# Kernel tuning notes

Hardware: AMD Instinct MI355X
Metric: run time of the kernel (lower is better)

## Reference

```python
import jax, jax.numpy as jnp
import numpy as np

NUM_HEADS = 16


def setup_inputs() -> dict:
    key = jax.random.key(0)
    ks = jax.random.split(key, 8)
    B, N, C = 2, 1024, 1024
    H, D = NUM_HEADS, C // NUM_HEADS
    Npast = 8192
    s = 0.02
    return {
        "x": jax.random.normal(ks[0], (B, N, C), jnp.float32),
        "past_k": jax.random.normal(ks[1], (B, H, Npast, D), jnp.float32),
        "past_v": jax.random.normal(ks[2], (B, H, Npast, D), jnp.float32),
        "qkv_w": jax.random.normal(ks[3], (3 * C, C), jnp.float32) * s,
        "qkv_b": jax.random.normal(ks[4], (3 * C,), jnp.float32) * s,
        "proj_w": jax.random.normal(ks[5], (C, C), jnp.float32) * s,
        "proj_b": jax.random.normal(ks[6], (C,), jnp.float32) * s,
        "cache_budget": 4096,
    }


def reference(x, past_k, past_v, qkv_w, qkv_b, proj_w, proj_b, cache_budget):
    B, N, C = x.shape
    H = NUM_HEADS
    D = C // H
    scale = D ** -0.5

    # fused QKV projection -> [3, B, H, N, D]
    qkv = (x @ qkv_w.T + qkv_b).reshape(B, N, 3, H, D).transpose(2, 0, 3, 1, 4)
    q, k, v = qkv[0], qkv[1], qkv[2]

    # use_cache path: anchor tokens = current-frame token count on first call
    num_anchor = N
    k = jnp.concatenate([past_k, k], axis=2)  # [B,H,Ntot,D]
    v = jnp.concatenate([past_v, v], axis=2)
    Ntot = k.shape[2]

    # eviction: mean cosine-similarity scoring over candidate (non-anchor) keys.
    # mean_j cos(k_i, k_j) == khat_i . mean_j(khat_j) -- O(N*D), no NxN matrix.
    num_keep = cache_budget - num_anchor
    cand_k = k[:, :, num_anchor:, :]  # [B,H,Ncand,D]
    khat = cand_k / (jnp.linalg.norm(cand_k, axis=-1, keepdims=True) + 1e-6)
    mean_dir = khat.mean(axis=2, keepdims=True)
    mean_scores = (khat * mean_dir).sum(-1)  # [B,H,Ncand]
    # keep the least-redundant tokens (lowest mean similarity)
    _, top_idx = jax.lax.top_k(-mean_scores, num_keep)  # [B,H,num_keep]
    top_idx = jnp.sort(top_idx, axis=-1)
    avg_scores = mean_scores.mean()

    anchor_idx = jnp.broadcast_to(jnp.arange(num_anchor)[None, None, :], (B, H, num_anchor))
    keep_idx = jnp.concatenate([anchor_idx, top_idx + num_anchor], axis=2)  # [B,H,budget]
    gidx = keep_idx[..., None]
    k_new = jnp.take_along_axis(k, jnp.broadcast_to(gidx, (B, H, cache_budget, D)), axis=2)
    v_new = jnp.take_along_axis(v, jnp.broadcast_to(gidx, (B, H, cache_budget, D)), axis=2)

    # SDPA
    logits = jnp.einsum("bhqd,bhkd->bhqk", q, k_new) * scale
    attn = jax.nn.softmax(logits, axis=-1)
    o = jnp.einsum("bhqk,bhkd->bhqd", attn, v_new)
    o = o.transpose(0, 2, 1, 3).reshape(B, N, C)
    out = o @ proj_w.T + proj_b
    return out, k_new, v_new, avg_scores
```

## Files before the change

### kernel.cpp

```cpp
#include <hip/hip_runtime.h>
#include <hip/hip_bf16.h>
#include <math.h>

#define BB 2
#define HH 16
#define NN 1024
#define CC 1024
#define DD 64
#define NPAST 8192
#define NANCH 1024
#define CBUD 4096
#define NKEEP 3072
#define NCAND 8192
#define BH 32

#define TILEB 16384

#define OUT_SZ   (BB*NN*CC)
#define KNEW_OFF ((size_t)OUT_SZ)
#define KNEW_SZ  ((size_t)BH*CBUD*DD)
#define VNEW_OFF (KNEW_OFF + KNEW_SZ)
#define AVG_OFF  (VNEW_OFF + KNEW_SZ)

#define WS_KF   ((size_t)0)
#define WS_VF   ((size_t)2097152)
#define WS_VTS  ((size_t)0)
#define WS_XT   ((size_t)4194304)
#define WS_OT   ((size_t)4194304)
#define WS_WQVT ((size_t)5242880)
#define WS_WPT  ((size_t)5242880)
#define WS_QB   ((size_t)6291456)
#define WS_MD   ((size_t)7340032)
#define WS_SC   ((size_t)7342080)
#define WS_BS   ((size_t)7604224)
#define WS_SEL  ((size_t)7604288)
#define WS_MDP  ((size_t)7702592)
#define WS_BSP  ((size_t)7718976)

typedef __attribute__((ext_vector_type(8))) short short8;
typedef __attribute__((ext_vector_type(4))) float f32x4;

typedef unsigned int __attribute__((address_space(3))) lds_uint;
typedef unsigned int __attribute__((address_space(1))) glb_uint;

__device__ __forceinline__ void gload16(const void* g, void* l) {
    __builtin_amdgcn_global_load_lds((const glb_uint*)g, (lds_uint*)l, 16, 0, 0);
}

__device__ inline unsigned short f2bf(float f) {
    unsigned u = __float_as_uint(f);
    unsigned r = (u + 0x7FFFu + ((u >> 16) & 1u)) >> 16;
    return (unsigned short)r;
}
__device__ inline unsigned cvtpk(float a, float b) {
    __hip_bfloat162 h = __float22bfloat162_rn(make_float2(a, b));
    return *reinterpret_cast<unsigned*>(&h);
}
__device__ __forceinline__ float fexp2(float x) {
#if __has_builtin(__builtin_amdgcn_exp2f)
    return __builtin_amdgcn_exp2f(x);
#else
    return exp2f(x);
#endif
}

__global__ __launch_bounds__(256) void conv_tile(const float* __restrict__ src,
                                                 unsigned short* __restrict__ dst)
{
    int gid = blockIdx.x * 256 + threadIdx.x;
    int r = gid >> 7, k0 = (gid & 127) * 8;
    float4 a = *(const float4*)&src[(size_t)r * 1024 + k0];
    float4 b = *(const float4*)&src[(size_t)r * 1024 + k0 + 4];
    uint4 u;
    u.x = cvtpk(a.x, a.y); u.y = cvtpk(a.z, a.w);
    u.z = cvtpk(b.x, b.y); u.w = cvtpk(b.z, b.w);
    size_t tile = (size_t)(r >> 7) * 16 + (k0 >> 6);
    int inner = (((r & 127) * 128 + (k0 & 63) * 2)) ^ ((r & 7) << 4);
    *(uint4*)((char*)dst + tile * TILEB + inner) = u;
}

__global__ __launch_bounds__(256) void conv_wqv(const float* __restrict__ src,
                                                unsigned short* __restrict__ dst)
{
    int gid = blockIdx.x * 256 + threadIdx.x;
    int n = gid >> 7, k0 = (gid & 127) * 8;
    int srow = (n < 1024) ? n : n + 1024;
    float4 a = *(const float4*)&src[(size_t)srow * 1024 + k0];
    float4 b = *(const float4*)&src[(size_t)srow * 1024 + k0 + 4];
    uint4 u;
    u.x = cvtpk(a.x, a.y); u.y = cvtpk(a.z, a.w);
    u.z = cvtpk(b.x, b.y); u.w = cvtpk(b.z, b.w);
    size_t tile = (size_t)(n >> 7) * 16 + (k0 >> 6);
    int inner = (((n & 127) * 128 + (k0 & 63) * 2)) ^ ((n & 7) << 4);
    *(uint4*)((char*)dst + tile * TILEB + inner) = u;
}

__global__ __launch_bounds__(256) void kf_gemm(const float* __restrict__ x,
                                               const float* __restrict__ w,
                                               const float* __restrict__ bias,
                                               float* __restrict__ ws)
{
    __shared__ float As[16][68];
    __shared__ float Bs[16][68];
    int tid = threadIdx.x;
    int m0 = blockIdx.y * 64;
    int n0 = blockIdx.x * 64;
    int tx = tid & 15, ty = tid >> 4;
    int lr = tid >> 2;
    int lk = (tid & 3) * 4;
    float acc[4][4] = {{0.f}};

    float4 a = *(const float4*)&x[(size_t)(m0 + lr) * CC + lk];
    float4 b = *(const float4*)&w[(size_t)(1024 + n0 + lr) * CC + lk];

    for (int k0 = 0; k0 < CC; k0 += 16) {
        __syncthreads();
        As[lk+0][lr] = a.x; As[lk+1][lr] = a.y; As[lk+2][lr] = a.z; As[lk+3][lr] = a.w;
        Bs[lk+0][lr] = b.x; Bs[lk+1][lr] = b.y; Bs[lk+2][lr] = b.z; Bs[lk+3][lr] = b.w;
        __syncthreads();
        if (k0 + 16 < CC) {
            a = *(const float4*)&x[(size_t)(m0 + lr) * CC + k0 + 16 + lk];
            b = *(const float4*)&w[(size_t)(1024 + n0 + lr) * CC + k0 + 16 + lk];
        }
        float tacc[4][4] = {{0.f}};
        #pragma unroll
        for (int kk = 0; kk < 16; ++kk) {
            float4 a4 = *(const float4*)&As[kk][ty*4];
            float4 b4 = *(const float4*)&Bs[kk][tx*4];
            float av[4] = {a4.x, a4.y, a4.z, a4.w};
            float bv[4] = {b4.x, b4.y, b4.z, b4.w};
            #pragma unroll
            for (int i = 0; i < 4; ++i)
                #pragma unroll
                for (int j = 0; j < 4; ++j)
                    tacc[i][j] += av[i] * bv[j];
        }
        #pragma unroll
        for (int i = 0; i < 4; ++i)
            #pragma unroll
            for (int j = 0; j < 4; ++j)
                acc[i][j] += tacc[i][j];
    }

    int cn0 = n0 + tx * 4;
    int h = cn0 >> 6, dd0 = cn0 & 63;
    float4 b4 = *(const float4*)&bias[1024 + cn0];
    float* kf = ws + WS_KF;
    #pragma unroll
    for (int i = 0; i < 4; ++i) {
        int m = m0 + ty * 4 + i;
        int b2 = m >> 10, n = m & 1023;
        float4 t;
        t.x = acc[i][0] + b4.x; t.y = acc[i][1] + b4.y;
        t.z = acc[i][2] + b4.z; t.w = acc[i][3] + b4.w;
        *(float4*)&kf[(((size_t)b2*HH + h)*NN + n)*DD + dd0] = t;
    }
}

template<int MODE>
__global__ __launch_bounds__(256) void mfma_gemm(const unsigned short* __restrict__ At,
                                                 const unsigned short* __restrict__ Bt,
                                                 const float* __restrict__ bias,
                                                 float* __restrict__ outp)
{
    __shared__ char lds[131072];
    int tid = threadIdx.x;
    int w = tid >> 6, lane = tid & 63;
    int g = lane >> 4, r16 = lane & 15;
    int wr = w >> 1, wc = w & 1;
    int bm = blockIdx.y, bn = blockIdx.x;
    const int KB = 16;
    const float QSCL = 0.125f * 1.44269504089f;

    f32x4 acc[4][4];
    #pragma unroll
    for (int i = 0; i < 4; ++i)
        #pragma unroll
        for (int j = 0; j < 4; ++j) acc[i][j] = 0.f;

    const char* Abase = (const char*)At + (size_t)bm * KB * TILEB;
    const char* Bbase = (const char*)Bt + (size_t)bn * KB * TILEB;

    #pragma unroll
    for (int i = 0; i < 4; ++i) {
        gload16(Abase + (size_t)w*4096 + i*1024 + lane*16, lds + w*4096 + i*1024);
        gload16(Bbase + (size_t)w*4096 + i*1024 + lane*16, lds + TILEB + w*4096 + i*1024);
    }
    asm volatile("s_waitcnt vmcnt(0)" ::: "memory");
    __syncthreads();

    int cur = 0;
    for (int kb = 0; kb < KB; ++kb) {
        char* Acur = lds + cur * (2*TILEB);
        char* Bcur = Acur + TILEB;
        if (kb + 1 < KB) {
            char* Anxt = lds + (cur ^ 1) * (2*TILEB);
            char* Bnxt = Anxt + TILEB;
            const char* an = Abase + (size_t)(kb+1)*TILEB + w*4096;
            const char* bsrc = Bbase + (size_t)(kb+1)*TILEB + w*4096;
            #pragma unroll
            for (int i = 0; i < 4; ++i) {
                gload16(an + i*1024 + lane*16, Anxt + w*4096 + i*1024);
                gload16(bsrc + i*1024 + lane*16, Bnxt + w*4096 + i*1024);
            }
        }
        short8 a0[4], a1[4], b0[4], b1[4];
        #pragma unroll
        for (int mi = 0; mi < 4; ++mi) {
            int row = wr*64 + mi*16 + r16;
            int sw = (row & 7) << 4;
            a0[mi] = *(const short8*)(Acur + ((row*128 + g*16) ^ sw));
            a1[mi] = *(const short8*)(Acur + ((row*128 + 64 + g*16) ^ sw));
        }
        #pragma unroll
        for (int ni = 0; ni < 4; ++ni) {
            int row = wc*64 + ni*16 + r16;
            int sw = (row & 7) << 4;
            b0[ni] = *(const short8*)(Bcur + ((row*128 + g*16) ^ sw));
            b1[ni] = *(const short8*)(Bcur + ((row*128 + 64 + g*16) ^ sw));
        }
        __builtin_amdgcn_s_setprio(1);
        #pragma unroll
        for (int mi = 0; mi < 4; ++mi)
            #pragma unroll
            for (int ni = 0; ni < 4; ++ni) {
                acc[mi][ni] = __builtin_amdgcn_mfma_f32_16x16x32_bf16(a0[mi], b0[ni], acc[mi][ni], 0, 0, 0);
                acc[mi][ni] = __builtin_amdgcn_mfma_f32_16x16x32_bf16(a1[mi], b1[ni], acc[mi][ni], 0, 0, 0);
            }
        __builtin_amdgcn_s_setprio(0);
        asm volatile("s_waitcnt vmcnt(0)" ::: "memory");
        __syncthreads();
        cur ^= 1;
    }

    int nq = bn*128 + wc*64;
    float bv[4];
    #pragma unroll
    for (int ni = 0; ni < 4; ++ni) {
        int n = nq + ni*16 + r16;
        bv[ni] = (MODE == 0) ? bias[(n < 1024) ? n : (n + 1024)] : bias[n];
    }
    #pragma unroll
    for (int mi = 0; mi < 4; ++mi) {
        #pragma unroll
        for (int rr = 0; rr < 4; ++rr) {
            int ml = wr*64 + mi*16 + 4*g + rr;
            int mg = bm*128 + ml;
            int bb = mg >> 10, tok = mg & 1023;
            #pragma unroll
            for (int ni = 0; ni < 4; ++ni) {
                int n = nq + ni*16 + r16;
                float v = acc[mi][ni][rr] + bv[ni];
                if (MODE == 0) {
                    if (n < 1024) {
                        unsigned short* qb = (unsigned short*)(outp + WS_QB);
                        int hh = n >> 6, d = n & 63;
                        qb[(((size_t)bb*16 + hh)*1024 + tok)*64 + d] = f2bf(v * QSCL);
                    } else {
                        float* vf = outp + WS_VF;
                        int hh = (n - 1024) >> 6, d = n & 63;
                        vf[(((size_t)bb*16 + hh)*1024 + tok)*64 + d] = v;
                    }
                } else {
                    outp[(size_t)mg*1024 + n] = v;
                }
            }
        }
    }
}

__global__ __launch_bounds__(256) void meandir_part(const float* __restrict__ past_k,
                                                    float* __restrict__ ws)
{
    int bh = blockIdx.x, seg = blockIdx.y, tid = threadIdx.x;
    const float* kpast = past_k + (size_t)bh * NPAST * DD;
    const float* knew  = ws + WS_KF + (size_t)bh * NN * DD;
    float dir[64];
    #pragma unroll
    for (int i = 0; i < 64; ++i) dir[i] = 0.f;

    int j0 = seg * 1024;
    for (int jj = tid; jj < 1024; jj += 256) {
        int pos = NANCH + j0 + jj;
        const float* row = (pos < NPAST) ? (kpast + (size_t)pos * DD)
                                         : (knew + (size_t)(pos - NPAST) * DD);
        float v[64]; float ss = 0.f;
        #pragma unroll
        for (int g = 0; g < 16; ++g) {
            float4 t = *(const float4*)&row[g*4];
            v[4*g]=t.x; v[4*g+1]=t.y; v[4*g+2]=t.z; v[4*g+3]=t.w;
            ss += t.x*t.x + t.y*t.y + t.z*t.z + t.w*t.w;
        }
        float inv = 1.0f / (sqrtf(ss) + 1e-6f);
        #pragma unroll
        for (int i = 0; i < 64; ++i) dir[i] += v[i] * inv;
    }
    #pragma unroll
    for (int i = 0; i < 64; ++i)
        for (int off = 32; off; off >>= 1) dir[i] += __shfl_xor(dir[i], off);

    __shared__ float sdir[4][64];
    int lane = tid & 63, wid = tid >> 6;
    if (lane == 0) {
        #pragma unroll
        for (int i = 0; i < 64; ++i) sdir[wid][i] = dir[i];
    }
    __syncthreads();
    if (tid < 64) {
        float s = sdir[0][tid] + sdir[1][tid] + sdir[2][tid] + sdir[3][tid];
        ws[WS_MDP + ((size_t)bh*8 + seg)*DD + tid] = s;
    }
}

__global__ void meandir_red(float* __restrict__ ws)
{
    int bh = blockIdx.x, tid = threadIdx.x;
    float s = 0.f;
    #pragma unroll
    for (int seg = 0; seg < 8; ++seg)
        s += ws[WS_MDP + ((size_t)bh*8 + seg)*DD + tid];
    ws[WS_MD + (size_t)bh*DD + tid] = s * (1.0f / (float)NCAND);
}

__global__ __launch_bounds__(256) void scores_part(const float* __restrict__ past_k,
                                                   float* __restrict__ ws)
{
    __shared__ float md[64];
    __shared__ float sred[4];
    int bh = blockIdx.x, seg = blockIdx.y, tid = threadIdx.x;
    if (tid < 64) md[tid] = ws[WS_MD + (size_t)bh*DD + tid];
    __syncthreads();
    const float* kpast = past_k + (size_t)bh * NPAST * DD;
    const float* knew  = ws + WS_KF + (size_t)bh * NN * DD;
    float ssum = 0.f;
    int j0 = seg * 1024;
    for (int jj = tid; jj < 1024; jj += 256) {
        int j = j0 + jj;
        int pos = NANCH + j;
        const float* row = (pos < NPAST) ? (kpast + (size_t)pos * DD)
                                         : (knew + (size_t)(pos - NPAST) * DD);
        float ss = 0.f, dp = 0.f;
        #pragma unroll
        for (int g = 0; g < 16; ++g) {
            float4 t = *(const float4*)&row[g*4];
            ss += t.x*t.x + t.y*t.y + t.z*t.z + t.w*t.w;
            dp += t.x*md[4*g] + t.y*md[4*g+1] + t.z*md[4*g+2] + t.w*md[4*g+3];
        }
        float sc = dp / (sqrtf(ss) + 1e-6f);
        ws[WS_SC + (size_t)bh*NCAND + j] = sc;
        ssum += sc;
    }
    for (int off = 32; off; off >>= 1) ssum += __shfl_xor(ssum, off);
    int lane = tid & 63, wid = tid >> 6;
    if (lane == 0) sred[wid] = ssum;
    __syncthreads();
    if (tid == 0)
        ws[WS_BSP + (size_t)bh*8 + seg] = sred[0] + sred[1] + sred[2] + sred[3];
}

__global__ void avg_k(const float* __restrict__ ws, float* __restrict__ dout)
{
    __shared__ float red[4];
    int tid = threadIdx.x;
    float v = ws[WS_BSP + tid];
    for (int off = 32; off; off >>= 1) v += __shfl_xor(v, off);
    int lane = tid & 63, wid = tid >> 6;
    if (lane == 0) red[wid] = v;
    __syncthreads();
    if (tid == 0)
        dout[AVG_OFF] = (red[0]+red[1]+red[2]+red[3]) * (1.0f / ((float)BH * (float)NCAND));
}

__global__ __launch_bounds__(1024) void topk_k(float* __restrict__ ws, int* __restrict__ sel)
{
    __shared__ unsigned keys[NCAND];
    __shared__ int hist[256];
    __shared__ int red[16];
    __shared__ int red2[16];
    __shared__ int bcast;
    __shared__ unsigned bbyte;
    int bh = blockIdx.x, tid = threadIdx.x;
    int lane = tid & 63, wid = tid >> 6;

    for (int j = tid; j < NCAND; j += 1024) {
        unsigned u = __float_as_uint(ws[WS_SC + (size_t)bh*NCAND + j]);
        u ^= (u & 0x80000000u) ? 0xFFFFFFFFu : 0x80000000u;
        keys[j] = u;
    }
    __syncthreads();

    int rem = NKEEP;
    unsigned prefix = 0;
    #pragma unroll
    for (int pass = 0; pass < 4; ++pass) {
        int shift = 24 - 8*pass;
        if (tid < 256) hist[tid] = 0;
        __syncthreads();
        unsigned himask = (pass == 0) ? 0u : (0xFFFFFFFFu << (shift + 8));
        for (int j = tid; j < NCAND; j += 1024) {
            unsigned k = keys[j];
            if ((k & himask) == prefix)
                atomicAdd(&hist[(k >> shift) & 255], 1);
        }
        __syncthreads();
        if (tid == 0) {
            int cum = 0, b = 0;
            for (; b < 255; ++b) {
                if (rem <= cum + hist[b]) break;
                cum += hist[b];
            }
            bcast = cum;
            bbyte = (unsigned)b;
        }
        __syncthreads();
        rem -= bcast;
        prefix |= (bbyte << shift);
        __syncthreads();
    }
    unsigned T = prefix;

    {
        int cnt = 0;
        for (int j = tid; j < NCAND; j += 1024) cnt += (int)(keys[j] < T);
        for (int off = 32; off; off >>= 1) cnt += __shfl_xor(cnt, off);
        if (lane == 0) red[wid] = cnt;
        __syncthreads();
        if (tid == 0) { int c = 0; for (int i = 0; i < 16; ++i) c += red[i]; bcast = c; }
        __syncthreads();
    }
    int c_less = bcast;
    int ttie = NKEEP - c_less;

    int base = tid * 8;
    unsigned kv[8]; int lcnt = 0, ecnt = 0;
    #pragma unroll
    for (int i = 0; i < 8; ++i) {
        kv[i] = keys[base + i];
        lcnt += (int)(kv[i] < T);
        ecnt += (int)(kv[i] == T);
    }
    int li = lcnt, ei = ecnt;
    for (int off = 1; off < 64; off <<= 1) {
        int tl = __shfl_up(li, off);
        int te = __shfl_up(ei, off);
        if (lane >= off) { li += tl; ei += te; }
    }
    __syncthreads();
    if (lane == 63) { red[wid] = li; red2[wid] = ei; }
    __syncthreads();
    int lb = 0, eb = 0;
    for (int w = 0; w < wid; ++w) { lb += red[w]; eb += red2[w]; }
    lb += li - lcnt; eb += ei - ecnt;
    #pragma unroll
    for (int i = 0; i < 8; ++i) {
        bool less = kv[i] < T, eq = kv[i] == T;
        if (less || (eq && eb < ttie)) {
            int pos = lb + (eb < ttie ? eb : ttie);
            sel[(size_t)bh*NKEEP + pos] = base + i;
        }
        lb += (int)less; eb += (int)eq;
    }
}

__global__ __launch_bounds__(256) void gather_k(const float* __restrict__ past_k,
                                                const float* __restrict__ past_v,
                                                const float* __restrict__ ws,
                                                const int* __restrict__ sel,
                                                float* __restrict__ dout)
{
    int gid = blockIdx.x * 256 + threadIdx.x;
    int row = gid >> 4, lane = gid & 15;
    int bh = row >> 12, r = row & 4095;
    int pos = (r < NANCH) ? r : (NANCH + sel[(size_t)bh*NKEEP + (r - NANCH)]);
    const float *kr, *vr;
    if (pos < NPAST) {
        kr = past_k + ((size_t)bh*NPAST + pos) * DD;
        vr = past_v + ((size_t)bh*NPAST + pos) * DD;
    } else {
        kr = ws + WS_KF + ((size_t)bh*NN + (pos - NPAST)) * DD;
        vr = ws + WS_VF + ((size_t)bh*NN + (pos - NPAST)) * DD;
    }
    float4 kq = *(const float4*)&kr[lane*4];
    float4 vq = *(const float4*)&vr[lane*4];
    *(float4*)&dout[KNEW_OFF + ((size_t)bh*CBUD + r)*DD + lane*4] = kq;
    *(float4*)&dout[VNEW_OFF + ((size_t)bh*CBUD + r)*DD + lane*4] = vq;
}

__global__ __launch_bounds__(256) void vtrans_k(const float* __restrict__ dout,
                                                unsigned short* __restrict__ vt)
{
    __shared__ unsigned short S[64][65];
    int bh = blockIdx.x >> 6, kt = blockIdx.x & 63;
    int c0 = kt * 64;
    int tid = threadIdx.x;
    int r = tid >> 2, c4 = (tid & 3) * 16;
    const float* src = dout + VNEW_OFF + ((size_t)bh*CBUD + c0 + r)*DD + c4;
    #pragma unroll
    for (int i = 0; i < 4; ++i) {
        float4 f = *(const float4*)&src[i*4];
        S[r][c4 + i*4 + 0] = f2bf(f.x);
        S[r][c4 + i*4 + 1] = f2bf(f.y);
        S[r][c4 + i*4 + 2] = f2bf(f.z);
        S[r][c4 + i*4 + 3] = f2bf(f.w);
    }
    __syncthreads();
    int d = r, k4 = c4;
    uint4 u0, u1;
    u0.x = (unsigned)S[k4+0][d] | ((unsigned)S[k4+1][d] << 16);
    u0.y = (unsigned)S[k4+2][d] | ((unsigned)S[k4+3][d] << 16);
    u0.z = (unsigned)S[k4+4][d] | ((unsigned)S[k4+5][d] << 16);
    u0.w = (unsigned)S[k4+6][d] | ((unsigned)S[k4+7][d] << 16);
    u1.x = (unsigned)S[k4+8][d] | ((unsigned)S[k4+9][d] << 16);
    u1.y = (unsigned)S[k4+10][d] | ((unsigned)S[k4+11][d] << 16);
    u1.z = (unsigned)S[k4+12][d] | ((unsigned)S[k4+13][d] << 16);
    u1.w = (unsigned)S[k4+14][d] | ((unsigned)S[k4+15][d] << 16);
    size_t tbase = ((size_t)bh*64 + kt) * 8192;
    int sw = (d & 7) << 4;
    *(uint4*)((char*)vt + tbase + ((d*128 + k4*2)      ^ sw)) = u0;
    *(uint4*)((char*)vt + tbase + ((d*128 + k4*2 + 16) ^ sw)) = u1;
}

__global__ __launch_bounds__(256) void attn_mfma(const unsigned short* __restrict__ qb,
                                                 const float* __restrict__ dout,
                                                 const unsigned short* __restrict__ vt,
                                                 unsigned short* __restrict__ ot)
{
    __shared__ char kls[2][8192];
    __shared__ char vls[2][8192];
    __shared__ char pls[4][2048];

    int orig = blockIdx.x;
    int bid = (orig & 7) * 64 + (orig >> 3);
    int bh = bid >> 4, qt = bid & 15;
    int b = bh >> 4, h = bh & 15;
    int tid = threadIdx.x;
    int w = tid >> 6, lane = tid & 63;
    int g = lane >> 4, r16 = lane & 15;
    int q0 = qt * 64 + w * 16;

    const unsigned short* qrow = qb + ((size_t)bh*NN + q0 + r16) * DD;
    short8 qa0 = *(const short8*)&qrow[8*g];
    short8 qa1 = *(const short8*)&qrow[32 + 8*g];

    const float* kf = dout + KNEW_OFF + (size_t)bh * CBUD * DD;
    const char* vtt = (const char*)vt + (size_t)bh * 64 * 8192;
    char* plw = pls[w];
    int psw = (r16 & 7) << 4;

    int srA = tid >> 3;
    int srB = srA + 32;
    int scb = (tid & 7) * 16;
    int d0  = scb >> 1;
    int sdA = (srA*128 + scb) ^ ((srA & 7) << 4);
    int sdB = (srB*128 + scb) ^ ((srB & 7) << 4);

    f32x4 accd[4];
    #pragma unroll
    for (int dt = 0; dt < 4; ++dt) accd[dt] = 0.f;
    float lsum = 0.f;

    {
        gload16(vtt + tid*16,        vls[0] + tid*16);
        gload16(vtt + 4096 + tid*16, vls[0] + 4096 + tid*16);
        const float* ksA = kf + (size_t)srA * DD + d0;
        const float* ksB = kf + (size_t)srB * DD + d0;
        float4 a0 = *(const float4*)ksA, a1 = *(const float4*)(ksA + 4);
        float4 b0 = *(const float4*)ksB, b1 = *(const float4*)(ksB + 4);
        uint4 kuA, kuB;
        kuA.x = cvtpk(a0.x,a0.y); kuA.y = cvtpk(a0.z,a0.w);
        kuA.z = cvtpk(a1.x,a1.y); kuA.w = cvtpk(a1.z,a1.w);
        kuB.x = cvtpk(b0.x,b0.y); kuB.y = cvtpk(b0.z,b0.w);
        kuB.z = cvtpk(b1.x,b1.y); kuB.w = cvtpk(b1.z,b1.w);
        *(uint4*)&kls[0][sdA] = kuA; *(uint4*)&kls[0][sdB] = kuB;
    }
    __syncthreads();

    int cur = 0;
    for (int t = 0; t < 64; ++t) {
        float4 a0, a1, b0, b1;
        bool more = (t + 1 < 64);
        if (more) {
            gload16(vtt + (size_t)(t+1)*8192 + tid*16,        vls[cur^1] + tid*16);
            gload16(vtt + (size_t)(t+1)*8192 + 4096 + tid*16, vls[cur^1] + 4096 + tid*16);
            const float* ksA = kf + ((size_t)(t+1)*64 + srA) * DD + d0;
            const float* ksB = kf + ((size_t)(t+1)*64 + srB) * DD + d0;
            a0 = *(const float4*)ksA; a1 = *(const float4*)(ksA + 4);
            b0 = *(const float4*)ksB; b1 = *(const float4*)(ksB + 4);
        }

        const char* kb = kls[cur];
        f32x4 sacc[4];
        #pragma unroll
        for (int t4 = 0; t4 < 4; ++t4) sacc[t4] = 0.f;
        __builtin_amdgcn_s_setprio(1);
        #pragma unroll
        for (int t4 = 0; t4 < 4; ++t4) {
            int row = 16*t4 + r16;
            int sw = (r16 & 7) << 4;
            short8 ka0 = *(const short8*)(kb + ((row*128 + g*16) ^ sw));
            short8 ka1 = *(const short8*)(kb + ((row*128 + 64 + g*16) ^ sw));
            sacc[t4] = __builtin_amdgcn_mfma_f32_16x16x32_bf16(ka0, qa0, sacc[t4], 0, 0, 0);
            sacc[t4] = __builtin_amdgcn_mfma_f32_16x16x32_bf16(ka1, qa1, sacc[t4], 0, 0, 0);
        }
        __builtin_amdgcn_s_setprio(0);

        float p[4][4];
        float ps = 0.f;
        #pragma unroll
        for (int t4 = 0; t4 < 4; ++t4) {
            p[t4][0] = fexp2(sacc[t4][0]);
            p[t4][1] = fexp2(sacc[t4][1]);
            p[t4][2] = fexp2(sacc[t4][2]);
            p[t4][3] = fexp2(sacc[t4][3]);
            ps += (p[t4][0] + p[t4][1]) + (p[t4][2] + p[t4][3]);
        }
        lsum += ps;
        #pragma unroll
        for (int t4 = 0; t4 < 4; ++t4) {
            uint2 u;
            u.x = cvtpk(p[t4][0], p[t4][1]);
            u.y = cvtpk(p[t4][2], p[t4][3]);
            int cb = (16*t4 + 4*g) * 2;
            *(uint2*)&plw[(r16*128 + cb) ^ psw] = u;
        }

        short8 pa0 = *(const short8*)&plw[(r16*128 + 16*g)      ^ psw];
        short8 pa1 = *(const short8*)&plw[(r16*128 + 64 + 16*g) ^ psw];
        const char* vb = vls[cur];
        __builtin_amdgcn_s_setprio(1);
        #pragma unroll
        for (int dt = 0; dt < 4; ++dt) {
            int row = dt*16 + r16;
            int sw = (r16 & 7) << 4;
            short8 vb0 = *(const short8*)(vb + ((row*128 + g*16) ^ sw));
            short8 vb1 = *(const short8*)(vb + ((row*128 + 64 + g*16) ^ sw));
            accd[dt] = __builtin_amdgcn_mfma_f32_16x16x32_bf16(pa0, vb0, accd[dt], 0, 0, 0);
            accd[dt] = __builtin_amdgcn_mfma_f32_16x16x32_bf16(pa1, vb1, accd[dt], 0, 0, 0);
        }
        __builtin_amdgcn_s_setprio(0);

        if (more) {
            uint4 kuA, kuB;
            kuA.x = cvtpk(a0.x,a0.y); kuA.y = cvtpk(a0.z,a0.w);
            kuA.z = cvtpk(a1.x,a1.y); kuA.w = cvtpk(a1.z,a1.w);
            kuB.x = cvtpk(b0.x,b0.y); kuB.y = cvtpk(b0.z,b0.w);
            kuB.z = cvtpk(b1.x,b1.y); kuB.w = cvtpk(b1.z,b1.w);
            *(uint4*)&kls[cur^1][sdA] = kuA; *(uint4*)&kls[cur^1][sdB] = kuB;
        }
        __syncthreads();
        cur ^= 1;
    }

    lsum += __shfl_xor(lsum, 16);
    lsum += __shfl_xor(lsum, 32);
    float ivl = 1.0f / lsum;
    float iq[4];
    #pragma unroll
    for (int rr = 0; rr < 4; ++rr) iq[rr] = __shfl(ivl, 20*g + rr);
    #pragma unroll
    for (int dt = 0; dt < 4; ++dt) {
        #pragma unroll
        for (int rr = 0; rr < 4; ++rr) {
            int q = q0 + 4*g + rr;
            int mrow = b*1024 + q;
            int d = dt*16 + r16;
            size_t tile = (size_t)(mrow >> 7) * 16 + h;
            int inner = ((mrow & 127)*128 + d*2) ^ ((mrow & 7) << 4);
            *(unsigned short*)((char*)ot + tile*TILEB + inner) = f2bf(accd[dt][rr] * iq[rr]);
        }
    }
}

extern "C" void kernel_launch(void* const* d_in, const int* in_sizes, int n_in,
                              void* d_out, int out_size, void* d_ws, size_t ws_size,
                              hipStream_t stream)
{
    (void)in_sizes; (void)n_in; (void)out_size; (void)ws_size;
    const float* x      = (const float*)d_in[0];
    const float* past_k = (const float*)d_in[1];
    const float* past_v = (const float*)d_in[2];
    const float* qkv_w  = (const float*)d_in[3];
    const float* qkv_b  = (const float*)d_in[4];
    const float* proj_w = (const float*)d_in[5];
    const float* proj_b = (const float*)d_in[6];
    float* out = (float*)d_out;
    float* ws  = (float*)d_ws;
    int*   sel = (int*)(ws + WS_SEL);
    unsigned short* xt   = (unsigned short*)(ws + WS_XT);
    unsigned short* wqvt = (unsigned short*)(ws + WS_WQVT);
    unsigned short* wpt  = (unsigned short*)(ws + WS_WPT);
    unsigned short* qbp  = (unsigned short*)(ws + WS_QB);
    unsigned short* vtp  = (unsigned short*)(ws + WS_VTS);
    unsigned short* otp  = (unsigned short*)(ws + WS_OT);

    conv_tile<<<1024, 256, 0, stream>>>(x, xt);
    conv_wqv<<<1024, 256, 0, stream>>>(qkv_w, wqvt);
    kf_gemm<<<dim3(16, 32), 256, 0, stream>>>(x, qkv_w, qkv_b, ws);
    mfma_gemm<0><<<dim3(16, 16), 256, 0, stream>>>(xt, wqvt, qkv_b, ws);
    meandir_part<<<dim3(32, 8), 256, 0, stream>>>(past_k, ws);
    meandir_red<<<32, 64, 0, stream>>>(ws);
    scores_part<<<dim3(32, 8), 256, 0, stream>>>(past_k, ws);
    avg_k<<<1, 256, 0, stream>>>(ws, out);
    topk_k<<<32, 1024, 0, stream>>>(ws, sel);
    gather_k<<<8192, 256, 0, stream>>>(past_k, past_v, ws, sel, out);
    vtrans_k<<<2048, 256, 0, stream>>>(out, vtp);
    conv_tile<<<512, 256, 0, stream>>>(proj_w, wpt);
    attn_mfma<<<512, 256, 0, stream>>>(qbp, out, vtp, otp);
    mfma_gemm<1><<<dim3(8, 16), 256, 0, stream>>>(otp, wpt, proj_b, out);
}
```

Before: 296.1 us.

## Merge small conversion kernels, fold avg into topk, double-buffer kf_gemm and attention tiles

Merges the x and weight bf16 conversion kernels into one launch, folds the avg-score reduction into block 0 of topk, and fuses the proj_w conversion into the V-transpose launch. This cuts the number of kernel launches. kf_gemm now double-buffers its shared tiles so each k-step needs one barrier instead of two. The attention kernel processes two 64-key tiles per loop iteration with doubled LDS buffers, which halves the barrier count but raises LDS use and may lower occupancy.

```diff
diff --git a/kernel.cpp b/kernel.cpp
--- a/kernel.cpp
+++ b/kernel.cpp
@@ -64,13 +64,21 @@
 #endif
 }
 
-__global__ __launch_bounds__(256) void conv_tile(const float* __restrict__ src,
-                                                 unsigned short* __restrict__ dst)
-{
-    int gid = blockIdx.x * 256 + threadIdx.x;
+__global__ __launch_bounds__(256) void conv_xw(const float* __restrict__ x,
+                                               const float* __restrict__ qw,
+                                               unsigned short* __restrict__ xt,
+                                               unsigned short* __restrict__ wqvt)
+{
+    int bid = blockIdx.x;
+    int gid = (bid & 1023) * 256 + threadIdx.x;
     int r = gid >> 7, k0 = (gid & 127) * 8;
-    float4 a = *(const float4*)&src[(size_t)r * 1024 + k0];
-    float4 b = *(const float4*)&src[(size_t)r * 1024 + k0 + 4];
+    const float* src;
+    unsigned short* dst;
+    int srow;
+    if (bid < 1024) { src = x;  dst = xt;   srow = r; }
+    else            { src = qw; dst = wqvt; srow = (r < 1024) ? r : r + 1024; }
+    float4 a = *(const float4*)&src[(size_t)srow * 1024 + k0];
+    float4 b = *(const float4*)&src[(size_t)srow * 1024 + k0 + 4];
     uint4 u;
     u.x = cvtpk(a.x, a.y); u.y = cvtpk(a.z, a.w);
     u.z = cvtpk(b.x, b.y); u.w = cvtpk(b.z, b.w);
@@ -79,29 +87,13 @@
     *(uint4*)((char*)dst + tile * TILEB + inner) = u;
 }
 
-__global__ __launch_bounds__(256) void conv_wqv(const float* __restrict__ src,
-                                                unsigned short* __restrict__ dst)
-{
-    int gid = blockIdx.x * 256 + threadIdx.x;
-    int n = gid >> 7, k0 = (gid & 127) * 8;
-    int srow = (n < 1024) ? n : n + 1024;
-    float4 a = *(const float4*)&src[(size_t)srow * 1024 + k0];
-    float4 b = *(const float4*)&src[(size_t)srow * 1024 + k0 + 4];
-    uint4 u;
-    u.x = cvtpk(a.x, a.y); u.y = cvtpk(a.z, a.w);
-    u.z = cvtpk(b.x, b.y); u.w = cvtpk(b.z, b.w);
-    size_t tile = (size_t)(n >> 7) * 16 + (k0 >> 6);
-    int inner = (((n & 127) * 128 + (k0 & 63) * 2)) ^ ((n & 7) << 4);
-    *(uint4*)((char*)dst + tile * TILEB + inner) = u;
-}
-
 __global__ __launch_bounds__(256) void kf_gemm(const float* __restrict__ x,
                                                const float* __restrict__ w,
                                                const float* __restrict__ bias,
                                                float* __restrict__ ws)
 {
-    __shared__ float As[16][68];
-    __shared__ float Bs[16][68];
+    __shared__ float As[2][16][68];
+    __shared__ float Bs[2][16][68];
     int tid = threadIdx.x;
     int m0 = blockIdx.y * 64;
     int n0 = blockIdx.x * 64;
@@ -110,23 +102,27 @@
     int lk = (tid & 3) * 4;
     float acc[4][4] = {{0.f}};
 
-    float4 a = *(const float4*)&x[(size_t)(m0 + lr) * CC + lk];
-    float4 b = *(const float4*)&w[(size_t)(1024 + n0 + lr) * CC + lk];
-
+    {
+        float4 a = *(const float4*)&x[(size_t)(m0 + lr) * CC + lk];
+        float4 b = *(const float4*)&w[(size_t)(1024 + n0 + lr) * CC + lk];
+        As[0][lk+0][lr] = a.x; As[0][lk+1][lr] = a.y; As[0][lk+2][lr] = a.z; As[0][lk+3][lr] = a.w;
+        Bs[0][lk+0][lr] = b.x; Bs[0][lk+1][lr] = b.y; Bs[0][lk+2][lr] = b.z; Bs[0][lk+3][lr] = b.w;
+    }
+    __syncthreads();
+
+    int cur = 0;
     for (int k0 = 0; k0 < CC; k0 += 16) {
-        __syncthreads();
-        As[lk+0][lr] = a.x; As[lk+1][lr] = a.y; As[lk+2][lr] = a.z; As[lk+3][lr] = a.w;
-        Bs[lk+0][lr] = b.x; Bs[lk+1][lr] = b.y; Bs[lk+2][lr] = b.z; Bs[lk+3][lr] = b.w;
-        __syncthreads();
-        if (k0 + 16 < CC) {
+        float4 a, b;
+        bool more = (k0 + 16 < CC);
+        if (more) {
             a = *(const float4*)&x[(size_t)(m0 + lr) * CC + k0 + 16 + lk];
             b = *(const float4*)&w[(size_t)(1024 + n0 + lr) * CC + k0 + 16 + lk];
         }
         float tacc[4][4] = {{0.f}};
         #pragma unroll
         for (int kk = 0; kk < 16; ++kk) {
-            float4 a4 = *(const float4*)&As[kk][ty*4];
-            float4 b4 = *(const float4*)&Bs[kk][tx*4];
+            float4 a4 = *(const float4*)&As[cur][kk][ty*4];
+            float4 b4 = *(const float4*)&Bs[cur][kk][tx*4];
             float av[4] = {a4.x, a4.y, a4.z, a4.w};
             float bv[4] = {b4.x, b4.y, b4.z, b4.w};
             #pragma unroll
@@ -140,6 +136,14 @@
             #pragma unroll
             for (int j = 0; j < 4; ++j)
                 acc[i][j] += tacc[i][j];
+        if (more) {
+            As[cur^1][lk+0][lr] = a.x; As[cur^1][lk+1][lr] = a.y;
+            As[cur^1][lk+2][lr] = a.z; As[cur^1][lk+3][lr] = a.w;
+            Bs[cur^1][lk+0][lr] = b.x; Bs[cur^1][lk+1][lr] = b.y;
+            Bs[cur^1][lk+2][lr] = b.z; Bs[cur^1][lk+3][lr] = b.w;
+        }
+        __syncthreads();
+        cur ^= 1;
     }
 
     int cn0 = n0 + tx * 4;
@@ -358,29 +362,31 @@
         ws[WS_BSP + (size_t)bh*8 + seg] = sred[0] + sred[1] + sred[2] + sred[3];
 }
 
-__global__ void avg_k(const float* __restrict__ ws, float* __restrict__ dout)
-{
-    __shared__ float red[4];
-    int tid = threadIdx.x;
-    float v = ws[WS_BSP + tid];
-    for (int off = 32; off; off >>= 1) v += __shfl_xor(v, off);
-    int lane = tid & 63, wid = tid >> 6;
-    if (lane == 0) red[wid] = v;
-    __syncthreads();
-    if (tid == 0)
-        dout[AVG_OFF] = (red[0]+red[1]+red[2]+red[3]) * (1.0f / ((float)BH * (float)NCAND));
-}
-
-__global__ __launch_bounds__(1024) void topk_k(float* __restrict__ ws, int* __restrict__ sel)
+__global__ __launch_bounds__(1024) void topk_k(float* __restrict__ ws, int* __restrict__ sel,
+                                               float* __restrict__ dout)
 {
     __shared__ unsigned keys[NCAND];
     __shared__ int hist[256];
     __shared__ int red[16];
     __shared__ int red2[16];
+    __shared__ float fred[16];
     __shared__ int bcast;
     __shared__ unsigned bbyte;
     int bh = blockIdx.x, tid = threadIdx.x;
     int lane = tid & 63, wid = tid >> 6;
+
+    if (bh == 0) {
+        float v = (tid < 256) ? ws[WS_BSP + tid] : 0.f;
+        for (int off = 32; off; off >>= 1) v += __shfl_xor(v, off);
+        if (lane == 0) fred[wid] = v;
+        __syncthreads();
+        if (tid == 0) {
+            float s = 0.f;
+            for (int i = 0; i < 16; ++i) s += fred[i];
+            dout[AVG_OFF] = s * (1.0f / ((float)BH * (float)NCAND));
+        }
+        __syncthreads();
+    }
 
     for (int j = tid; j < NCAND; j += 1024) {
         unsigned u = __float_as_uint(ws[WS_SC + (size_t)bh*NCAND + j]);
@@ -486,9 +492,24 @@
     *(float4*)&dout[VNEW_OFF + ((size_t)bh*CBUD + r)*DD + lane*4] = vq;
 }
 
-__global__ __launch_bounds__(256) void vtrans_k(const float* __restrict__ dout,
-                                                unsigned short* __restrict__ vt)
-{
+__global__ __launch_bounds__(256) void vtrans_conv(const float* __restrict__ dout,
+                                                   unsigned short* __restrict__ vt,
+                                                   const float* __restrict__ pw,
+                                                   unsigned short* __restrict__ wpt)
+{
+    if (blockIdx.x >= 2048) {
+        int gid = (blockIdx.x - 2048) * 256 + threadIdx.x;
+        int r = gid >> 7, k0 = (gid & 127) * 8;
+        float4 a = *(const float4*)&pw[(size_t)r * 1024 + k0];
+        float4 b = *(const float4*)&pw[(size_t)r * 1024 + k0 + 4];
+        uint4 u;
+        u.x = cvtpk(a.x, a.y); u.y = cvtpk(a.z, a.w);
+        u.z = cvtpk(b.x, b.y); u.w = cvtpk(b.z, b.w);
+        size_t tile = (size_t)(r >> 7) * 16 + (k0 >> 6);
+        int inner = (((r & 127) * 128 + (k0 & 63) * 2)) ^ ((r & 7) << 4);
+        *(uint4*)((char*)wpt + tile * TILEB + inner) = u;
+        return;
+    }
     __shared__ unsigned short S[64][65];
     int bh = blockIdx.x >> 6, kt = blockIdx.x & 63;
     int c0 = kt * 64;
@@ -525,8 +546,8 @@
                                                  const unsigned short* __restrict__ vt,
                                                  unsigned short* __restrict__ ot)
 {
-    __shared__ char kls[2][8192];
-    __shared__ char vls[2][8192];
+    __shared__ char kls[2][2][8192];
+    __shared__ char vls[2][2][8192];
     __shared__ char pls[4][2048];
 
     int orig = blockIdx.x;
@@ -560,92 +581,111 @@
     float lsum = 0.f;
 
     {
-        gload16(vtt + tid*16,        vls[0] + tid*16);
-        gload16(vtt + 4096 + tid*16, vls[0] + 4096 + tid*16);
-        const float* ksA = kf + (size_t)srA * DD + d0;
-        const float* ksB = kf + (size_t)srB * DD + d0;
-        float4 a0 = *(const float4*)ksA, a1 = *(const float4*)(ksA + 4);
-        float4 b0 = *(const float4*)ksB, b1 = *(const float4*)(ksB + 4);
-        uint4 kuA, kuB;
-        kuA.x = cvtpk(a0.x,a0.y); kuA.y = cvtpk(a0.z,a0.w);
-        kuA.z = cvtpk(a1.x,a1.y); kuA.w = cvtpk(a1.z,a1.w);
-        kuB.x = cvtpk(b0.x,b0.y); kuB.y = cvtpk(b0.z,b0.w);
-        kuB.z = cvtpk(b1.x,b1.y); kuB.w = cvtpk(b1.z,b1.w);
-        *(uint4*)&kls[0][sdA] = kuA; *(uint4*)&kls[0][sdB] = kuB;
-    }
-    __syncthreads();
-
-    int cur = 0;
-    for (int t = 0; t < 64; ++t) {
-        float4 a0, a1, b0, b1;
-        bool more = (t + 1 < 64);
-        if (more) {
-            gload16(vtt + (size_t)(t+1)*8192 + tid*16,        vls[cur^1] + tid*16);
-            gload16(vtt + (size_t)(t+1)*8192 + 4096 + tid*16, vls[cur^1] + 4096 + tid*16);
-            const float* ksA = kf + ((size_t)(t+1)*64 + srA) * DD + d0;
-            const float* ksB = kf + ((size_t)(t+1)*64 + srB) * DD + d0;
-            a0 = *(const float4*)ksA; a1 = *(const float4*)(ksA + 4);
-            b0 = *(const float4*)ksB; b1 = *(const float4*)(ksB + 4);
-        }
-
-        const char* kb = kls[cur];
-        f32x4 sacc[4];
-        #pragma unroll
-        for (int t4 = 0; t4 < 4; ++t4) sacc[t4] = 0.f;
-        __builtin_amdgcn_s_setprio(1);
-        #pragma unroll
-        for (int t4 = 0; t4 < 4; ++t4) {
-            int row = 16*t4 + r16;
-            int sw = (r16 & 7) << 4;
-            short8 ka0 = *(const short8*)(kb + ((row*128 + g*16) ^ sw));
-            short8 ka1 = *(const short8*)(kb + ((row*128 + 64 + g*16) ^ sw));
-            sacc[t4] = __builtin_amdgcn_mfma_f32_16x16x32_bf16(ka0, qa0, sacc[t4], 0, 0, 0);
-            sacc[t4] = __builtin_amdgcn_mfma_f32_16x16x32_bf16(ka1, qa1, sacc[t4], 0, 0, 0);
-        }
-        __builtin_amdgcn_s_setprio(0);
-
-        float p[4][4];
-        float ps = 0.f;
-        #pragma unroll
-        for (int t4 = 0; t4 < 4; ++t4) {
-            p[t4][0] = fexp2(sacc[t4][0]);
-            p[t4][1] = fexp2(sacc[t4][1]);
-            p[t4][2] = fexp2(sacc[t4][2]);
-            p[t4][3] = fexp2(sacc[t4][3]);
-            ps += (p[t4][0] + p[t4][1]) + (p[t4][2] + p[t4][3]);
-        }
-        lsum += ps;
-        #pragma unroll
-        for (int t4 = 0; t4 < 4; ++t4) {
-            uint2 u;
-            u.x = cvtpk(p[t4][0], p[t4][1]);
-            u.y = cvtpk(p[t4][2], p[t4][3]);
-            int cb = (16*t4 + 4*g) * 2;
-            *(uint2*)&plw[(r16*128 + cb) ^ psw] = u;
-        }
-
-        short8 pa0 = *(const short8*)&plw[(r16*128 + 16*g)      ^ psw];
-        short8 pa1 = *(const short8*)&plw[(r16*128 + 64 + 16*g) ^ psw];
-        const char* vb = vls[cur];
-        __builtin_amdgcn_s_setprio(1);
-        #pragma unroll
-        for (int dt = 0; dt < 4; ++dt) {
-            int row = dt*16 + r16;
-            int sw = (r16 & 7) << 4;
-            short8 vb0 = *(const short8*)(vb + ((row*128 + g*16) ^ sw));
-            short8 vb1 = *(const short8*)(vb + ((row*128 + 64 + g*16) ^ sw));
-            accd[dt] = __builtin_amdgcn_mfma_f32_16x16x32_bf16(pa0, vb0, accd[dt], 0, 0, 0);
-            accd[dt] = __builtin_amdgcn_mfma_f32_16x16x32_bf16(pa1, vb1, accd[dt], 0, 0, 0);
-        }
-        __builtin_amdgcn_s_setprio(0);
-
-        if (more) {
+        gload16(vtt + tid*16,               vls[0][0] + tid*16);
+        gload16(vtt + 4096 + tid*16,        vls[0][0] + 4096 + tid*16);
+        gload16(vtt + 8192 + tid*16,        vls[0][1] + tid*16);
+        gload16(vtt + 8192 + 4096 + tid*16, vls[0][1] + 4096 + tid*16);
+        #pragma unroll
+        for (int hh = 0; hh < 2; ++hh) {
+            const float* ksA = kf + ((size_t)hh*64 + srA) * DD + d0;
+            const float* ksB = kf + ((size_t)hh*64 + srB) * DD + d0;
+            float4 a0 = *(const float4*)ksA, a1 = *(const float4*)(ksA + 4);
+            float4 b0 = *(const float4*)ksB, b1 = *(const float4*)(ksB + 4);
             uint4 kuA, kuB;
             kuA.x = cvtpk(a0.x,a0.y); kuA.y = cvtpk(a0.z,a0.w);
             kuA.z = cvtpk(a1.x,a1.y); kuA.w = cvtpk(a1.z,a1.w);
             kuB.x = cvtpk(b0.x,b0.y); kuB.y = cvtpk(b0.z,b0.w);
             kuB.z = cvtpk(b1.x,b1.y); kuB.w = cvtpk(b1.z,b1.w);
-            *(uint4*)&kls[cur^1][sdA] = kuA; *(uint4*)&kls[cur^1][sdB] = kuB;
+            *(uint4*)&kls[0][hh][sdA] = kuA;
+            *(uint4*)&kls[0][hh][sdB] = kuB;
+        }
+    }
+    __syncthreads();
+
+    int cur = 0;
+    for (int t = 0; t < 32; ++t) {
+        float4 na0[2], na1[2], nb0[2], nb1[2];
+        bool more = (t + 1 < 32);
+        if (more) {
+            int nt = 2*t + 2;
+            gload16(vtt + (size_t)nt*8192 + tid*16,            vls[cur^1][0] + tid*16);
+            gload16(vtt + (size_t)nt*8192 + 4096 + tid*16,     vls[cur^1][0] + 4096 + tid*16);
+            gload16(vtt + (size_t)(nt+1)*8192 + tid*16,        vls[cur^1][1] + tid*16);
+            gload16(vtt + (size_t)(nt+1)*8192 + 4096 + tid*16, vls[cur^1][1] + 4096 + tid*16);
+            #pragma unroll
+            for (int hh = 0; hh < 2; ++hh) {
+                const float* ksA = kf + ((size_t)(nt+hh)*64 + srA) * DD + d0;
+                const float* ksB = kf + ((size_t)(nt+hh)*64 + srB) * DD + d0;
+                na0[hh] = *(const float4*)ksA; na1[hh] = *(const float4*)(ksA + 4);
+                nb0[hh] = *(const float4*)ksB; nb1[hh] = *(const float4*)(ksB + 4);
+            }
+        }
+
+        #pragma unroll
+        for (int hh = 0; hh < 2; ++hh) {
+            const char* kb = kls[cur][hh];
+            f32x4 sacc[4];
+            #pragma unroll
+            for (int t4 = 0; t4 < 4; ++t4) sacc[t4] = 0.f;
+            __builtin_amdgcn_s_setprio(1);
+            #pragma unroll
+            for (int t4 = 0; t4 < 4; ++t4) {
+                int row = 16*t4 + r16;
+                int sw = (r16 & 7) << 4;
+                short8 ka0 = *(const short8*)(kb + ((row*128 + g*16) ^ sw));
+                short8 ka1 = *(const short8*)(kb + ((row*128 + 64 + g*16) ^ sw));
+                sacc[t4] = __builtin_amdgcn_mfma_f32_16x16x32_bf16(ka0, qa0, sacc[t4], 0, 0, 0);
+                sacc[t4] = __builtin_amdgcn_mfma_f32_16x16x32_bf16(ka1, qa1, sacc[t4], 0, 0, 0);
+            }
+            __builtin_amdgcn_s_setprio(0);
+
+            float p[4][4];
+            float ps = 0.f;
+            #pragma unroll
+            for (int t4 = 0; t4 < 4; ++t4) {
+                p[t4][0] = fexp2(sacc[t4][0]);
+                p[t4][1] = fexp2(sacc[t4][1]);
+                p[t4][2] = fexp2(sacc[t4][2]);
+                p[t4][3] = fexp2(sacc[t4][3]);
+                ps += (p[t4][0] + p[t4][1]) + (p[t4][2] + p[t4][3]);
+            }
+            lsum += ps;
+            #pragma unroll
+            for (int t4 = 0; t4 < 4; ++t4) {
+                uint2 u;
+                u.x = cvtpk(p[t4][0], p[t4][1]);
+                u.y = cvtpk(p[t4][2], p[t4][3]);
+                int cb = (16*t4 + 4*g) * 2;
+                *(uint2*)&plw[(r16*128 + cb) ^ psw] = u;
+            }
+
+            short8 pa0 = *(const short8*)&plw[(r16*128 + 16*g)      ^ psw];
+            short8 pa1 = *(const short8*)&plw[(r16*128 + 64 + 16*g) ^ psw];
+            const char* vb = vls[cur][hh];
+            __builtin_amdgcn_s_setprio(1);
+            #pragma unroll
+            for (int dt = 0; dt < 4; ++dt) {
+                int row = dt*16 + r16;
+                int sw = (r16 & 7) << 4;
+                short8 vb0 = *(const short8*)(vb + ((row*128 + g*16) ^ sw));
+                short8 vb1 = *(const short8*)(vb + ((row*128 + 64 + g*16) ^ sw));
+                accd[dt] = __builtin_amdgcn_mfma_f32_16x16x32_bf16(pa0, vb0, accd[dt], 0, 0, 0);
+                accd[dt] = __builtin_amdgcn_mfma_f32_16x16x32_bf16(pa1, vb1, accd[dt], 0, 0, 0);
+            }
+            __builtin_amdgcn_s_setprio(0);
+        }
+
+        if (more) {
+            #pragma unroll
+            for (int hh = 0; hh < 2; ++hh) {
+                uint4 kuA, kuB;
+                kuA.x = cvtpk(na0[hh].x, na0[hh].y); kuA.y = cvtpk(na0[hh].z, na0[hh].w);
+                kuA.z = cvtpk(na1[hh].x, na1[hh].y); kuA.w = cvtpk(na1[hh].z, na1[hh].w);
+                kuB.x = cvtpk(nb0[hh].x, nb0[hh].y); kuB.y = cvtpk(nb0[hh].z, nb0[hh].w);
+                kuB.z = cvtpk(nb1[hh].x, nb1[hh].y); kuB.w = cvtpk(nb1[hh].z, nb1[hh].w);
+                *(uint4*)&kls[cur^1][hh][sdA] = kuA;
+                *(uint4*)&kls[cur^1][hh][sdB] = kuB;
+            }
         }
         __syncthreads();
         cur ^= 1;
@@ -693,18 +733,15 @@
     unsigned short* vtp  = (unsigned short*)(ws + WS_VTS);
     unsigned short* otp  = (unsigned short*)(ws + WS_OT);
 
-    conv_tile<<<1024, 256, 0, stream>>>(x, xt);
-    conv_wqv<<<1024, 256, 0, stream>>>(qkv_w, wqvt);
+    conv_xw<<<2048, 256, 0, stream>>>(x, qkv_w, xt, wqvt);
     kf_gemm<<<dim3(16, 32), 256, 0, stream>>>(x, qkv_w, qkv_b, ws);
     mfma_gemm<0><<<dim3(16, 16), 256, 0, stream>>>(xt, wqvt, qkv_b, ws);
     meandir_part<<<dim3(32, 8), 256, 0, stream>>>(past_k, ws);
     meandir_red<<<32, 64, 0, stream>>>(ws);
     scores_part<<<dim3(32, 8), 256, 0, stream>>>(past_k, ws);
-    avg_k<<<1, 256, 0, stream>>>(ws, out);
-    topk_k<<<32, 1024, 0, stream>>>(ws, sel);
+    topk_k<<<32, 1024, 0, stream>>>(ws, sel, out);
     gather_k<<<8192, 256, 0, stream>>>(past_k, past_v, ws, sel, out);
-    vtrans_k<<<2048, 256, 0, stream>>>(out, vtp);
-    conv_tile<<<512, 256, 0, stream>>>(proj_w, wpt);
+    vtrans_conv<<<2560, 256, 0, stream>>>(out, vtp, proj_w, wpt);
     attn_mfma<<<512, 256, 0, stream>>>(qbp, out, vtp, otp);
     mfma_gemm<1><<<dim3(8, 16), 256, 0, stream>>>(otp, wpt, proj_b, out);
 }
```

Result: faster. 283.7 us (-4.2%).
